# Optimization experiments

Hardware: AMD Instinct MI355X
Metric: run time of the kernel (lower is better)

The kernel has to match this reference:

```python
import jax, jax.numpy as jnp
import numpy as np


def euler_xyz_to_matrix(angles):
    # pytorch3d euler_angles_to_matrix(angles, 'XYZ') = R_X(a0) @ R_Y(a1) @ R_Z(a2)
    ax, ay, az = angles[..., 0], angles[..., 1], angles[..., 2]
    cx, sx = jnp.cos(ax), jnp.sin(ax)
    cy, sy = jnp.cos(ay), jnp.sin(ay)
    cz, sz = jnp.cos(az), jnp.sin(az)
    one = jnp.ones_like(ax)
    zero = jnp.zeros_like(ax)
    Rx = jnp.stack([one, zero, zero, zero, cx, -sx, zero, sx, cx], axis=-1).reshape(*ax.shape, 3, 3)
    Ry = jnp.stack([cy, zero, sy, zero, one, zero, -sy, zero, cy], axis=-1).reshape(*ax.shape, 3, 3)
    Rz = jnp.stack([cz, -sz, zero, sz, cz, zero, zero, zero, one], axis=-1).reshape(*ax.shape, 3, 3)
    return Rx @ Ry @ Rz


def chamfer_bidir(x, y):
    # x, y: [R, I, N, 3]. Squared-distance chamfer, mean point reduction, per (R,I) batch.
    x2 = jnp.sum(x * x, axis=-1)  # [R,I,N]
    y2 = jnp.sum(y * y, axis=-1)  # [R,I,N]
    # d2[r,i,n,m] = |x_n - y_m|^2
    d2 = x2[..., :, None] + y2[..., None, :] - 2.0 * jnp.einsum('rind,rimd->rinm', x, y)
    cham_x = jnp.mean(jnp.min(d2, axis=-1), axis=-1)  # x -> nearest y
    cham_y = jnp.mean(jnp.min(d2, axis=-2), axis=-1)  # y -> nearest x
    return cham_x + cham_y  # [R, I]


def setup_inputs() -> dict:
    key = jax.random.key(0)
    k1, k2, k3, k4 = jax.random.split(key, 4)
    R, I, N = 4, 16, 2048
    source_points = jax.random.normal(k1, (R, I, N, 3), dtype=jnp.float32)
    target_points = jax.random.normal(k2, (I, N, 3), dtype=jnp.float32)
    rotation = 0.1 * jax.random.normal(k3, (R, I, 3), dtype=jnp.float32)
    translation = 0.1 * jax.random.normal(k4, (R, I, 3), dtype=jnp.float32)
    scale = jnp.ones((R, I), dtype=jnp.float32)
    return {
        'source_points': source_points,
        'target_points': target_points,
        'rotation': rotation,
        'translation': translation,
        'scale': scale,
    }


def reference(source_points, target_points, rotation, translation, scale):
    R, I, N, _ = source_points.shape
    rot = euler_xyz_to_matrix(rotation)  # [R,I,3,3]
    # Transform per original: 4x4 matrix with rows [:3,:] scaled by `scale`,
    # so p' = scale * (rot @ p + translation).
    transformed = scale[..., None, None] * (
        jnp.einsum('rind,rikd->rink', source_points, rot) + translation[..., None, :]
    )  # [R,I,N,3]
    # target_points [I,N,3] broadcast to [R,I,N,3] (original repeats along R)
    target = jnp.broadcast_to(target_points[None], transformed.shape)
    # original calls chamfer_distance(target, transformed): x=target, y=transformed
    return chamfer_bidir(target, transformed)  # [R, I]
```

## Files before the change

kernel.cpp:

```cpp
#include <hip/hip_runtime.h>
#include <math.h>

#define RDIM 4
#define IDIM 16
#define NPAIR 64
#define NPTS 2048
#define THREADS 256
#define ROWSB 256
#define RBLK (NPTS / ROWSB)
#define TILES (NPTS / 32)
#define PSPLIT 4
#define ONEBF 0x3F80u

typedef __attribute__((ext_vector_type(8))) short bf16x8;
typedef __attribute__((ext_vector_type(16))) float f32x16;
typedef __attribute__((ext_vector_type(4))) float f32x4;

__device__ __forceinline__ float min3f(float a, float b, float c) {
    return fminf(a, fminf(b, c));
}

__device__ __forceinline__ unsigned int f2bf(float f) {
    union { float f; unsigned int u; } v; v.f = f;
    return (v.u + 0x7FFFu + ((v.u >> 16) & 1u)) >> 16;
}
__device__ __forceinline__ float bf2f(unsigned int h) {
    union { unsigned int u; float f; } v; v.u = h << 16; return v.f;
}

__device__ __forceinline__ void make_rot(const float* __restrict__ rotv, int pair,
                                         float& r00, float& r01, float& r02,
                                         float& r10, float& r11, float& r12,
                                         float& r20, float& r21, float& r22) {
    const float ax = rotv[pair * 3 + 0];
    const float ay = rotv[pair * 3 + 1];
    const float az = rotv[pair * 3 + 2];
    float sx, cx, sy, cy, sz, cz;
    sincosf(ax, &sx, &cx);
    sincosf(ay, &sy, &cy);
    sincosf(az, &sz, &cz);
    r00 = cy * cz;                r01 = -cy * sz;               r02 = sy;
    r10 = cx * sz + sx * sy * cz; r11 = cx * cz - sx * sy * sz; r12 = -sx * cy;
    r20 = sx * sz - cx * sy * cz; r21 = sx * cz + cx * sy * sz; r22 = cx * cy;
}

__device__ __forceinline__ uint4 brec(float v0, float v1, float v2) {
    const float b0 = -2.0f * v0, b1 = -2.0f * v1, b2 = -2.0f * v2;
    const unsigned int h0 = f2bf(b0), h1 = f2bf(b1), h2 = f2bf(b2);
    const unsigned int l0 = f2bf(b0 - bf2f(h0));
    const unsigned int l1 = f2bf(b1 - bf2f(h1));
    const unsigned int l2 = f2bf(b2 - bf2f(h2));
    const float n2 = v0 * v0 + v1 * v1 + v2 * v2;
    const unsigned int nh = f2bf(n2), nl = f2bf(n2 - bf2f(nh));
    return make_uint4(h0 | (h1 << 16), h2 | (l0 << 16), l1 | (l2 << 16), nh | (nl << 16));
}
__device__ __forceinline__ void arec(float q0, float q1, float q2, uint4& a0, uint4& a1) {
    const unsigned int h0 = f2bf(q0), h1 = f2bf(q1), h2 = f2bf(q2);
    const unsigned int l0 = f2bf(q0 - bf2f(h0));
    const unsigned int l1 = f2bf(q1 - bf2f(h1));
    const unsigned int l2 = f2bf(q2 - bf2f(h2));
    a0 = make_uint4(h0 | (h1 << 16), h2 | (l0 << 16), l1 | (l2 << 16), ONEBF);
    a1 = make_uint4(l0 | (l1 << 16), l2 | (h0 << 16), h1 | (h2 << 16), ONEBF << 16);
}

__global__ __launch_bounds__(THREADS)
void prep(const float* __restrict__ src, const float* __restrict__ tgt,
          const float* __restrict__ rotv, const float* __restrict__ trav,
          const float* __restrict__ scal,
          uint4* __restrict__ Yb, uint4* __restrict__ Ya,
          uint4* __restrict__ Xb, uint4* __restrict__ Xa,
          float* __restrict__ out)
{
    const int b   = blockIdx.x;
    const int seg = blockIdx.y;
    const int tid = threadIdx.x;
    if (b == 0 && seg == 0 && tid < NPAIR) out[tid] = 0.0f;
    const int m0  = seg * (NPTS / PSPLIT);
    if (b < NPAIR) {
        const int pair = b;
        float r00, r01, r02, r10, r11, r12, r20, r21, r22;
        make_rot(rotv, pair, r00, r01, r02, r10, r11, r12, r20, r21, r22);
        const float t0 = trav[pair * 3 + 0];
        const float t1 = trav[pair * 3 + 1];
        const float t2 = trav[pair * 3 + 2];
        const float s  = scal[pair];
        const float* __restrict__ srcp = src + (size_t)pair * NPTS * 3;
#pragma unroll
        for (int u = 0; u < NPTS / THREADS / PSPLIT; ++u) {
            const int m = m0 + u * THREADS + tid;
            const float p0 = srcp[m * 3 + 0];
            const float p1 = srcp[m * 3 + 1];
            const float p2 = srcp[m * 3 + 2];
            const float y0 = s * fmaf(r00, p0, fmaf(r01, p1, fmaf(r02, p2, t0)));
            const float y1 = s * fmaf(r10, p0, fmaf(r11, p1, fmaf(r12, p2, t1)));
            const float y2 = s * fmaf(r20, p0, fmaf(r21, p1, fmaf(r22, p2, t2)));
            Yb[(size_t)pair * NPTS + m] = brec(y0, y1, y2);
            uint4 a0, a1;
            arec(y0, y1, y2, a0, a1);
            Ya[((size_t)pair * NPTS + m) * 2 + 0] = a0;
            Ya[((size_t)pair * NPTS + m) * 2 + 1] = a1;
        }
    } else {
        const int i = b - NPAIR;
        const float* __restrict__ tgtp = tgt + (size_t)i * NPTS * 3;
#pragma unroll
        for (int u = 0; u < NPTS / THREADS / PSPLIT; ++u) {
            const int m = m0 + u * THREADS + tid;
            const float x0 = tgtp[m * 3 + 0];
            const float x1 = tgtp[m * 3 + 1];
            const float x2 = tgtp[m * 3 + 2];
            Xb[(size_t)i * NPTS + m] = brec(x0, x1, x2);
            uint4 a0, a1;
            arec(x0, x1, x2, a0, a1);
            Xa[((size_t)i * NPTS + m) * 2 + 0] = a0;
            Xa[((size_t)i * NPTS + m) * 2 + 1] = a1;
        }
    }
}

__global__ __launch_bounds__(THREADS, 3)
void chamfer_main(const uint4* __restrict__ Yb, const uint4* __restrict__ Ya,
                  const uint4* __restrict__ Xb, const uint4* __restrict__ Xa,
                  float* __restrict__ out, const float czero)
{
    __shared__ alignas(16) unsigned char smem[32768];
    __shared__ float rowmin[ROWSB];
    __shared__ float wsum[4];
    unsigned short* sB = (unsigned short*)smem;

    const int pair  = blockIdx.x;
    const int rb    = blockIdx.y;
    const int passB = blockIdx.z;
    const int i     = pair & (IDIM - 1);
    const int tid   = threadIdx.x;
    const int lane  = tid & 63;
    const int w     = tid >> 6;
    const int c31   = lane & 31;
    const int h     = lane >> 5;

    const uint4* __restrict__ gB = (passB == 0) ? (Yb + (size_t)pair * NPTS)
                                                : (Xb + (size_t)i * NPTS);
    const uint4* __restrict__ gA = (passB == 0)
        ? (Xa + ((size_t)i * NPTS + rb * ROWSB) * 2)
        : (Ya + ((size_t)pair * NPTS + rb * ROWSB) * 2);
    const char* gAb = (const char*)gA;

#pragma unroll
    for (int j = 0; j < 8; ++j)
        ((uint4*)sB)[j * THREADS + tid] = gB[j * THREADS + tid];

    const bf16x8 af0 = *(const bf16x8*)(gAb + (w * 64 + c31) * 32 + h * 16);
    const bf16x8 af1 = *(const bf16x8*)(gAb + (w * 64 + 32 + c31) * 32 + h * 16);

    f32x16 czv;
#pragma unroll
    for (int j = 0; j < 16; ++j) czv[j] = czero;

    float mn0[16], mn1[16];
#pragma unroll
    for (int j = 0; j < 16; ++j) { mn0[j] = 3.4e38f; mn1[j] = 3.4e38f; }

    __syncthreads();

    for (int t = 0; t < TILES; t += 2) {
        const bf16x8 bfA = *(const bf16x8*)&sB[((t + 0) * 32 + c31) * 8];
        const bf16x8 bfB = *(const bf16x8*)&sB[((t + 1) * 32 + c31) * 8];
        {
            const f32x16 a0 = __builtin_amdgcn_mfma_f32_32x32x16_bf16(af0, bfA, czv, 0, 0, 0);
            const f32x16 b0 = __builtin_amdgcn_mfma_f32_32x32x16_bf16(af0, bfB, czv, 0, 0, 0);
#pragma unroll
            for (int j = 0; j < 16; ++j)
                mn0[j] = min3f(mn0[j], a0[j], b0[j]);
        }
        {
            const f32x16 a1 = __builtin_amdgcn_mfma_f32_32x32x16_bf16(af1, bfA, czv, 0, 0, 0);
            const f32x16 b1 = __builtin_amdgcn_mfma_f32_32x32x16_bf16(af1, bfB, czv, 0, 0, 0);
#pragma unroll
            for (int j = 0; j < 16; ++j)
                mn1[j] = min3f(mn1[j], a1[j], b1[j]);
        }
    }

#pragma unroll
    for (int j = 0; j < 16; ++j) {
        float v0 = mn0[j], v1 = mn1[j];
        v0 = fminf(v0, __shfl_xor(v0, 1, 64));
        v1 = fminf(v1, __shfl_xor(v1, 1, 64));
        v0 = fminf(v0, __shfl_xor(v0, 2, 64));
        v1 = fminf(v1, __shfl_xor(v1, 2, 64));
        v0 = fminf(v0, __shfl_xor(v0, 4, 64));
        v1 = fminf(v1, __shfl_xor(v1, 4, 64));
        v0 = fminf(v0, __shfl_xor(v0, 8, 64));
        v1 = fminf(v1, __shfl_xor(v1, 8, 64));
        v0 = fminf(v0, __shfl_xor(v0, 16, 64));
        v1 = fminf(v1, __shfl_xor(v1, 16, 64));
        mn0[j] = v0; mn1[j] = v1;
    }

    if (c31 == 0) {
#pragma unroll
        for (int g = 0; g < 4; ++g) {
            f32x4 v4, u4;
            v4[0] = mn0[g * 4 + 0]; v4[1] = mn0[g * 4 + 1];
            v4[2] = mn0[g * 4 + 2]; v4[3] = mn0[g * 4 + 3];
            u4[0] = mn1[g * 4 + 0]; u4[1] = mn1[g * 4 + 1];
            u4[2] = mn1[g * 4 + 2]; u4[3] = mn1[g * 4 + 3];
            *(f32x4*)&rowmin[w * 64 + 8 * g + 4 * h] = v4;
            *(f32x4*)&rowmin[w * 64 + 32 + 8 * g + 4 * h] = u4;
        }
    }
    __syncthreads();

    const float m = rowmin[tid];
    const unsigned short* ar = (const unsigned short*)(gAb + tid * 32);
    const float q0 = bf2f(ar[0]) + bf2f(ar[3]);
    const float q1 = bf2f(ar[1]) + bf2f(ar[4]);
    const float q2 = bf2f(ar[2]) + bf2f(ar[5]);
    float v = m + q0 * q0 + q1 * q1 + q2 * q2;

#pragma unroll
    for (int off = 32; off > 0; off >>= 1)
        v += __shfl_down(v, off, 64);
    if (lane == 0) wsum[w] = v;
    __syncthreads();
    if (tid == 0) {
        const float tot = wsum[0] + wsum[1] + wsum[2] + wsum[3];
        atomicAdd(&out[pair], tot * (1.0f / NPTS));
    }
}

extern "C" void kernel_launch(void* const* d_in, const int* in_sizes, int n_in,
                              void* d_out, int out_size, void* d_ws, size_t ws_size,
                              hipStream_t stream) {
    const float* src  = (const float*)d_in[0];
    const float* tgt  = (const float*)d_in[1];
    const float* rotv = (const float*)d_in[2];
    const float* trav = (const float*)d_in[3];
    const float* scal = (const float*)d_in[4];
    float* out = (float*)d_out;

    char* ws = (char*)d_ws;
    uint4* Yb = (uint4*)ws;
    uint4* Ya = (uint4*)(ws + (size_t)NPAIR * NPTS * 16);
    uint4* Xb = (uint4*)(ws + (size_t)NPAIR * NPTS * 48);
    uint4* Xa = (uint4*)(ws + (size_t)NPAIR * NPTS * 48 + (size_t)IDIM * NPTS * 16);

    dim3 pgrid(NPAIR + IDIM, PSPLIT);
    prep<<<pgrid, THREADS, 0, stream>>>(src, tgt, rotv, trav, scal, Yb, Ya, Xb, Xa, out);

    dim3 grid(NPAIR, RBLK, 2);
    chamfer_main<<<grid, THREADS, 0, stream>>>(Yb, Ya, Xb, Xa, out, 0.0f);
}
```

Before: 88.97 us.

## Double rows per block and software-pipeline MFMA with min reductions

Each wave now handles 128 query rows (four 32-row MFMA tiles) instead of 64, so every B fragment read from LDS feeds twice as many MFMAs and the block count halves. The main loop is software-pipelined so the min reduction of one tile overlaps the MFMAs of the next, with the B loads for the following tile pair issued early. Register pressure roughly doubles, so launch bounds drop to 2 blocks per SM, lowering occupancy and shrinking the grid.

```diff
diff --git a/kernel.cpp b/kernel.cpp
--- a/kernel.cpp
+++ b/kernel.cpp
@@ -6,7 +6,7 @@
 #define NPAIR 64
 #define NPTS 2048
 #define THREADS 256
-#define ROWSB 256
+#define ROWSB 512
 #define RBLK (NPTS / ROWSB)
 #define TILES (NPTS / 32)
 #define PSPLIT 4
@@ -118,7 +118,7 @@
     }
 }
 
-__global__ __launch_bounds__(THREADS, 3)
+__global__ __launch_bounds__(THREADS, 2)
 void chamfer_main(const uint4* __restrict__ Yb, const uint4* __restrict__ Ya,
                   const uint4* __restrict__ Xb, const uint4* __restrict__ Xa,
                   float* __restrict__ out, const float czero)
@@ -149,75 +149,88 @@
     for (int j = 0; j < 8; ++j)
         ((uint4*)sB)[j * THREADS + tid] = gB[j * THREADS + tid];
 
-    const bf16x8 af0 = *(const bf16x8*)(gAb + (w * 64 + c31) * 32 + h * 16);
-    const bf16x8 af1 = *(const bf16x8*)(gAb + (w * 64 + 32 + c31) * 32 + h * 16);
+    bf16x8 af[4];
+#pragma unroll
+    for (int rt = 0; rt < 4; ++rt)
+        af[rt] = *(const bf16x8*)(gAb + (w * 128 + rt * 32 + c31) * 32 + h * 16);
 
     f32x16 czv;
 #pragma unroll
     for (int j = 0; j < 16; ++j) czv[j] = czero;
 
-    float mn0[16], mn1[16];
-#pragma unroll
-    for (int j = 0; j < 16; ++j) { mn0[j] = 3.4e38f; mn1[j] = 3.4e38f; }
+    float mn[4][16];
+#pragma unroll
+    for (int rt = 0; rt < 4; ++rt)
+#pragma unroll
+        for (int j = 0; j < 16; ++j) mn[rt][j] = 3.4e38f;
 
     __syncthreads();
 
+    bf16x8 bfA = *(const bf16x8*)&sB[(0 * 32 + c31) * 8];
+    bf16x8 bfB = *(const bf16x8*)&sB[(1 * 32 + c31) * 8];
+    f32x16 x0a = __builtin_amdgcn_mfma_f32_32x32x16_bf16(af[0], bfA, czv, 0, 0, 0);
+    f32x16 x0b = __builtin_amdgcn_mfma_f32_32x32x16_bf16(af[0], bfB, czv, 0, 0, 0);
     for (int t = 0; t < TILES; t += 2) {
-        const bf16x8 bfA = *(const bf16x8*)&sB[((t + 0) * 32 + c31) * 8];
-        const bf16x8 bfB = *(const bf16x8*)&sB[((t + 1) * 32 + c31) * 8];
-        {
-            const f32x16 a0 = __builtin_amdgcn_mfma_f32_32x32x16_bf16(af0, bfA, czv, 0, 0, 0);
-            const f32x16 b0 = __builtin_amdgcn_mfma_f32_32x32x16_bf16(af0, bfB, czv, 0, 0, 0);
-#pragma unroll
-            for (int j = 0; j < 16; ++j)
-                mn0[j] = min3f(mn0[j], a0[j], b0[j]);
+        const f32x16 x1a = __builtin_amdgcn_mfma_f32_32x32x16_bf16(af[1], bfA, czv, 0, 0, 0);
+        const f32x16 x1b = __builtin_amdgcn_mfma_f32_32x32x16_bf16(af[1], bfB, czv, 0, 0, 0);
+#pragma unroll
+        for (int j = 0; j < 16; ++j)
+            mn[0][j] = min3f(mn[0][j], x0a[j], x0b[j]);
+        const f32x16 x2a = __builtin_amdgcn_mfma_f32_32x32x16_bf16(af[2], bfA, czv, 0, 0, 0);
+        const f32x16 x2b = __builtin_amdgcn_mfma_f32_32x32x16_bf16(af[2], bfB, czv, 0, 0, 0);
+#pragma unroll
+        for (int j = 0; j < 16; ++j)
+            mn[1][j] = min3f(mn[1][j], x1a[j], x1b[j]);
+        const f32x16 x3a = __builtin_amdgcn_mfma_f32_32x32x16_bf16(af[3], bfA, czv, 0, 0, 0);
+        const f32x16 x3b = __builtin_amdgcn_mfma_f32_32x32x16_bf16(af[3], bfB, czv, 0, 0, 0);
+#pragma unroll
+        for (int j = 0; j < 16; ++j)
+            mn[2][j] = min3f(mn[2][j], x2a[j], x2b[j]);
+        bfA = *(const bf16x8*)&sB[((((t + 2) & 63)) * 32 + c31) * 8];
+        bfB = *(const bf16x8*)&sB[((((t + 3) & 63)) * 32 + c31) * 8];
+        x0a = __builtin_amdgcn_mfma_f32_32x32x16_bf16(af[0], bfA, czv, 0, 0, 0);
+        x0b = __builtin_amdgcn_mfma_f32_32x32x16_bf16(af[0], bfB, czv, 0, 0, 0);
+#pragma unroll
+        for (int j = 0; j < 16; ++j)
+            mn[3][j] = min3f(mn[3][j], x3a[j], x3b[j]);
+    }
+
+#pragma unroll
+    for (int rt = 0; rt < 4; ++rt)
+#pragma unroll
+        for (int j = 0; j < 16; ++j) {
+            float v = mn[rt][j];
+            v = fminf(v, __shfl_xor(v, 1, 64));
+            v = fminf(v, __shfl_xor(v, 2, 64));
+            v = fminf(v, __shfl_xor(v, 4, 64));
+            v = fminf(v, __shfl_xor(v, 8, 64));
+            v = fminf(v, __shfl_xor(v, 16, 64));
+            mn[rt][j] = v;
         }
-        {
-            const f32x16 a1 = __builtin_amdgcn_mfma_f32_32x32x16_bf16(af1, bfA, czv, 0, 0, 0);
-            const f32x16 b1 = __builtin_amdgcn_mfma_f32_32x32x16_bf16(af1, bfB, czv, 0, 0, 0);
-#pragma unroll
-            for (int j = 0; j < 16; ++j)
-                mn1[j] = min3f(mn1[j], a1[j], b1[j]);
-        }
-    }
-
-#pragma unroll
-    for (int j = 0; j < 16; ++j) {
-        float v0 = mn0[j], v1 = mn1[j];
-        v0 = fminf(v0, __shfl_xor(v0, 1, 64));
-        v1 = fminf(v1, __shfl_xor(v1, 1, 64));
-        v0 = fminf(v0, __shfl_xor(v0, 2, 64));
-        v1 = fminf(v1, __shfl_xor(v1, 2, 64));
-        v0 = fminf(v0, __shfl_xor(v0, 4, 64));
-        v1 = fminf(v1, __shfl_xor(v1, 4, 64));
-        v0 = fminf(v0, __shfl_xor(v0, 8, 64));
-        v1 = fminf(v1, __shfl_xor(v1, 8, 64));
-        v0 = fminf(v0, __shfl_xor(v0, 16, 64));
-        v1 = fminf(v1, __shfl_xor(v1, 16, 64));
-        mn0[j] = v0; mn1[j] = v1;
-    }
 
     if (c31 == 0) {
 #pragma unroll
-        for (int g = 0; g < 4; ++g) {
-            f32x4 v4, u4;
-            v4[0] = mn0[g * 4 + 0]; v4[1] = mn0[g * 4 + 1];
-            v4[2] = mn0[g * 4 + 2]; v4[3] = mn0[g * 4 + 3];
-            u4[0] = mn1[g * 4 + 0]; u4[1] = mn1[g * 4 + 1];
-            u4[2] = mn1[g * 4 + 2]; u4[3] = mn1[g * 4 + 3];
-            *(f32x4*)&rowmin[w * 64 + 8 * g + 4 * h] = v4;
-            *(f32x4*)&rowmin[w * 64 + 32 + 8 * g + 4 * h] = u4;
-        }
+        for (int rt = 0; rt < 4; ++rt)
+#pragma unroll
+            for (int g = 0; g < 4; ++g) {
+                f32x4 v4;
+                v4[0] = mn[rt][g * 4 + 0]; v4[1] = mn[rt][g * 4 + 1];
+                v4[2] = mn[rt][g * 4 + 2]; v4[3] = mn[rt][g * 4 + 3];
+                *(f32x4*)&rowmin[w * 128 + rt * 32 + 8 * g + 4 * h] = v4;
+            }
     }
     __syncthreads();
 
-    const float m = rowmin[tid];
-    const unsigned short* ar = (const unsigned short*)(gAb + tid * 32);
-    const float q0 = bf2f(ar[0]) + bf2f(ar[3]);
-    const float q1 = bf2f(ar[1]) + bf2f(ar[4]);
-    const float q2 = bf2f(ar[2]) + bf2f(ar[5]);
-    float v = m + q0 * q0 + q1 * q1 + q2 * q2;
-
+    float v = 0.0f;
+#pragma unroll
+    for (int rr = 0; rr < 2; ++rr) {
+        const int row = rr * THREADS + tid;
+        const unsigned short* ar = (const unsigned short*)(gAb + row * 32);
+        const float q0 = bf2f(ar[0]) + bf2f(ar[3]);
+        const float q1 = bf2f(ar[1]) + bf2f(ar[4]);
+        const float q2 = bf2f(ar[2]) + bf2f(ar[5]);
+        v += rowmin[row] + q0 * q0 + q1 * q1 + q2 * q2;
+    }
 #pragma unroll
     for (int off = 32; off > 0; off >>= 1)
         v += __shfl_down(v, off, 64);
```

New measurement: 89.43 us. About the same (+0.5%).
